# Performance work log

Hardware: AMD Instinct MI355X
Metric: run time of the kernel (lower is better)

The kernel has to match this reference:

```python
import jax, jax.numpy as jnp
import numpy as np
import math

D_MODEL = 768
N_HEADS = 12
D_HEAD = D_MODEL // N_HEADS


def setup_inputs() -> dict:
    key = jax.random.key(0)
    ks = jax.random.split(key, 5)
    x = jax.random.normal(ks[0], (2, 4096, D_MODEL), dtype=jnp.float32)
    s = 1.0 / math.sqrt(D_MODEL)
    W_qkv = jax.random.normal(ks[1], (D_MODEL, 3 * D_MODEL), dtype=jnp.float32) * s
    b_qkv = jnp.zeros((3 * D_MODEL,), dtype=jnp.float32)
    W_out = jax.random.normal(ks[2], (D_MODEL, D_MODEL), dtype=jnp.float32) * s
    b_out = jnp.zeros((D_MODEL,), dtype=jnp.float32)
    return {"x": x, "W_qkv": W_qkv, "b_qkv": b_qkv, "W_out": W_out, "b_out": b_out}


def reference(x, W_qkv, b_qkv, W_out, b_out):
    B, T, C = x.shape
    H, Dh = N_HEADS, D_HEAD
    qkv = x @ W_qkv + b_qkv                      # [B,T,3C]
    q, k, v = jnp.split(qkv, 3, axis=-1)
    q = q.reshape(B, T, H, Dh).transpose(0, 2, 1, 3)  # [B,H,T,Dh]
    k = k.reshape(B, T, H, Dh).transpose(0, 2, 1, 3)
    v = v.reshape(B, T, H, Dh).transpose(0, 2, 1, 3)
    att = jnp.einsum('bhqd,bhkd->bhqk', q, k) * (1.0 / math.sqrt(Dh))
    causal = jnp.tril(jnp.ones((T, T), dtype=bool))
    att = jnp.where(causal, att, -jnp.inf)
    att = jax.nn.softmax(att, axis=-1)
    out = jnp.einsum('bhqk,bhkd->bhqd', att, v)  # [B,H,T,Dh]
    out = out.transpose(0, 2, 1, 3).reshape(B, T, C)
    return out @ W_out + b_out
```

## Files before the change

### kernel.cpp

```cpp
#include <hip/hip_runtime.h>
#include <hip/hip_bf16.h>
#include <cstdint>

#define NH 12
#define DH 64
#define TSEQ 4096
#define BATCH 2
#define CDIM 768
#define MROWS (BATCH*TSEQ)

typedef __bf16 bf16x8 __attribute__((ext_vector_type(8)));
typedef __bf16 bf16x4 __attribute__((ext_vector_type(4)));
typedef bf16x8 bf16x8_a __attribute__((may_alias));
typedef bf16x4 bf16x4_a __attribute__((may_alias));
typedef float f32x4 __attribute__((ext_vector_type(4)));

__device__ __forceinline__ uint16_t f2bu(float f) {
  uint32_t u = __float_as_uint(f);
  u += 0x7fffu + ((u >> 16) & 1u);
  return (uint16_t)(u >> 16);
}

__device__ __forceinline__ float bu2f(uint16_t x) {
  return __uint_as_float(((uint32_t)x) << 16);
}

__device__ __forceinline__ void gload_lds16(const void* g, void* l) {
  __builtin_amdgcn_global_load_lds(
      (const __attribute__((address_space(1))) void*)g,
      (__attribute__((address_space(3))) void*)l, 16, 0, 0);
}

__global__ void cast_f32_bf16(const float* __restrict__ in, uint16_t* __restrict__ out, int n4) {
  int i = blockIdx.x * blockDim.x + threadIdx.x;
  int stride = gridDim.x * blockDim.x;
  for (; i < n4; i += stride) {
    float4 v = ((const float4*)in)[i];
    ushort4 o;
    o.x = f2bu(v.x); o.y = f2bu(v.y); o.z = f2bu(v.z); o.w = f2bu(v.w);
    ((ushort4*)out)[i] = o;
  }
}

__global__ void transpose_cast(const float* __restrict__ w, uint16_t* __restrict__ wt, int K, int N) {
  __shared__ float tile[32][33];
  int kb = blockIdx.x * 32, nb = blockIdx.y * 32;
  int tx = threadIdx.x & 31, ty = threadIdx.x >> 5;
  #pragma unroll
  for (int r = ty; r < 32; r += 8) tile[r][tx] = w[(size_t)(kb + r) * N + nb + tx];
  __syncthreads();
  #pragma unroll
  for (int r = ty; r < 32; r += 8) wt[(size_t)(nb + r) * K + kb + tx] = f2bu(tile[tx][r]);
}

__global__ __launch_bounds__(256) void gemm_qkv(
    const uint16_t* __restrict__ A, const uint16_t* __restrict__ Bt,
    const float* __restrict__ bias,
    uint16_t* __restrict__ q, uint16_t* __restrict__ k, uint16_t* __restrict__ v,
    int N, int K) {
  __shared__ uint16_t As[128 * 32];
  __shared__ uint16_t Bs[128 * 32];
  int tid = threadIdx.x;
  int w = tid >> 6, l = tid & 63;
  int lg = l >> 4, lr = l & 15;
  int mb = blockIdx.x * 128, nb = blockIdx.y * 128;
  int wr = (w >> 1) * 64, wc = (w & 1) * 64;
  f32x4 acc[4][4] = {};
  int srow = tid >> 2, scol = (tid & 3) * 8;
  const uint16_t* Ag = A + (size_t)(mb + srow) * K + scol;
  const uint16_t* Bg = Bt + (size_t)(nb + srow) * K + scol;
  char* AsB = (char*)As + (size_t)w * 1024;
  char* BsB = (char*)Bs + (size_t)w * 1024;
  size_t rowskip = (size_t)64 * K;
  for (int kb = 0; kb < K; kb += 32) {
    __syncthreads();
    gload_lds16(Ag + kb, AsB);
    gload_lds16(Ag + kb + rowskip, AsB + 4096);
    gload_lds16(Bg + kb, BsB);
    gload_lds16(Bg + kb + rowskip, BsB + 4096);
    __syncthreads();
    bf16x8 af[4], bfr[4];
    #pragma unroll
    for (int i = 0; i < 4; ++i)
      af[i] = *(const bf16x8_a*)(const void*)(As + (wr + i * 16 + lr) * 32 + lg * 8);
    #pragma unroll
    for (int i = 0; i < 4; ++i)
      bfr[i] = *(const bf16x8_a*)(const void*)(Bs + (wc + i * 16 + lr) * 32 + lg * 8);
    #pragma unroll
    for (int mi = 0; mi < 4; ++mi)
      #pragma unroll
      for (int ni = 0; ni < 4; ++ni)
        acc[mi][ni] = __builtin_amdgcn_mfma_f32_16x16x32_bf16(af[mi], bfr[ni], acc[mi][ni], 0, 0, 0);
  }
  #pragma unroll
  for (int mi = 0; mi < 4; ++mi) {
    #pragma unroll
    for (int ni = 0; ni < 4; ++ni) {
      int gm0 = mb + wr + mi * 16 + lg * 4;
      int gn = nb + wc + ni * 16 + lr;
      int which = gn / CDIM;
      int cc = gn - which * CDIM;
      int hh = cc >> 6, d = cc & 63;
      float bs = bias[gn];
      if (which == 2) {
        int b0 = gm0 >> 12, t0 = gm0 & 4095;
        ushort4 pk;
        pk.x = f2bu(acc[mi][ni][0] + bs);
        pk.y = f2bu(acc[mi][ni][1] + bs);
        pk.z = f2bu(acc[mi][ni][2] + bs);
        pk.w = f2bu(acc[mi][ni][3] + bs);
        *(ushort4*)&v[(((size_t)(b0 * NH + hh)) * DH + d) * TSEQ + t0] = pk;
      } else {
        uint16_t* dst = which ? k : q;
        float sc = which ? 1.0f : 0.1803368801111204f;
        #pragma unroll
        for (int j = 0; j < 4; ++j) {
          int gm = gm0 + j;
          int bb = gm >> 12, t = gm & 4095;
          float val = (acc[mi][ni][j] + bs) * sc;
          dst[(((size_t)(bb * NH + hh)) * TSEQ + t) * DH + d] = f2bu(val);
        }
      }
    }
  }
}

__global__ __launch_bounds__(256) void gemm_out(
    const uint16_t* __restrict__ A, const uint16_t* __restrict__ Bt,
    const float* __restrict__ bias, float* __restrict__ outf, int N, int K) {
  __shared__ uint16_t As[128 * 32];
  __shared__ uint16_t Bs[64 * 32];
  int tid = threadIdx.x;
  int w = tid >> 6, l = tid & 63;
  int lg = l >> 4, lr = l & 15;
  int mb = blockIdx.x * 128, nb = blockIdx.y * 64;
  int wr = w * 32;
  f32x4 acc[2][4] = {};
  int srow = tid >> 2, scol = (tid & 3) * 8;
  const uint16_t* Ag = A + (size_t)(mb + srow) * K + scol;
  const uint16_t* Bg = Bt + (size_t)(nb + srow) * K + scol;
  char* AsB = (char*)As + (size_t)w * 1024;
  char* BsB = (char*)Bs + (size_t)w * 1024;
  size_t rowskip = (size_t)64 * K;
  for (int kb = 0; kb < K; kb += 32) {
    __syncthreads();
    gload_lds16(Ag + kb, AsB);
    gload_lds16(Ag + kb + rowskip, AsB + 4096);
    gload_lds16(Bg + kb, BsB);
    __syncthreads();
    bf16x8 af[2], bfr[4];
    #pragma unroll
    for (int i = 0; i < 2; ++i)
      af[i] = *(const bf16x8_a*)(const void*)(As + (wr + i * 16 + lr) * 32 + lg * 8);
    #pragma unroll
    for (int i = 0; i < 4; ++i)
      bfr[i] = *(const bf16x8_a*)(const void*)(Bs + (i * 16 + lr) * 32 + lg * 8);
    #pragma unroll
    for (int mi = 0; mi < 2; ++mi)
      #pragma unroll
      for (int ni = 0; ni < 4; ++ni)
        acc[mi][ni] = __builtin_amdgcn_mfma_f32_16x16x32_bf16(af[mi], bfr[ni], acc[mi][ni], 0, 0, 0);
  }
  #pragma unroll
  for (int mi = 0; mi < 2; ++mi) {
    #pragma unroll
    for (int ni = 0; ni < 4; ++ni) {
      #pragma unroll
      for (int j = 0; j < 4; ++j) {
        int gm = mb + wr + mi * 16 + lg * 4 + j;
        int gn = nb + ni * 16 + lr;
        outf[(size_t)gm * N + gn] = acc[mi][ni][j] + bias[gn];
      }
    }
  }
}

__device__ __forceinline__ int lbase_qt(int qt) {
  return (qt < 22) ? (qt - 11) * 2 : 22 + (qt - 22) * 3;
}
__device__ __forceinline__ int ebase_qt(int qt) {
  return (qt < 22) ? (qt - 11) : 11 + (qt - 22) * 2;
}

__global__ __launch_bounds__(256) void attn_part(
    const uint16_t* __restrict__ Q, const uint16_t* __restrict__ K,
    const uint16_t* __restrict__ Vt, uint16_t* __restrict__ O,
    uint16_t* __restrict__ Pbuf, float* __restrict__ Pl) {
  int gid = blockIdx.x;
  int widx = gid / 24, bh = gid - widx * 24;
  int qt, c, nch;
  if (widx < 30) { qt = 31 - widx / 3; c = widx % 3; nch = 3; }
  else if (widx < 52) { int u = widx - 30; qt = 21 - (u >> 1); c = u & 1; nch = 2; }
  else { qt = 62 - widx; c = 0; nch = 1; }
  int ntile = 2 * qt + 2;
  int L = (ntile + nch - 1) / nch;
  int t0 = c * L;
  int t1 = min(ntile - 1, t0 + L - 1);

  int b = bh / NH, hd = bh - b * NH;
  size_t base = (size_t)bh * TSEQ * DH;
  int tid = threadIdx.x, w = tid >> 6, lane = tid & 63;
  int lg = lane >> 4, lr = lane & 15;
  __shared__ __align__(16) uint16_t Ks[64 * 64];
  __shared__ __align__(16) uint16_t Vs[64 * 64];
  __shared__ uint16_t Ps[4][16 * 64];
  char* pw = (char*)Ps[w];
  int srow = tid >> 3;
  int schunk = (tid & 7) ^ (srow & 7);
  const uint16_t* Kg0 = K + base + (size_t)srow * DH + schunk * 8;
  const uint16_t* Vg0 = Vt + base + (size_t)srow * TSEQ + schunk * 8;
  char* KsB = (char*)Ks + w * 1024;
  char* VsB = (char*)Vs + w * 1024;
  int swzA = (lg ^ (lr & 7)) << 4;
  int swzB = swzA ^ 64;

  int qb = qt * 128;
  int qgA = qb + w * 16 + lr;
  int qgB = qgA + 64;
  bf16x8 qA0 = *(const bf16x8_a*)(const void*)(Q + base + (size_t)qgA * DH + lg * 8);
  bf16x8 qA1 = *(const bf16x8_a*)(const void*)(Q + base + (size_t)qgA * DH + 32 + lg * 8);
  bf16x8 qB0 = *(const bf16x8_a*)(const void*)(Q + base + (size_t)qgB * DH + lg * 8);
  bf16x8 qB1 = *(const bf16x8_a*)(const void*)(Q + base + (size_t)qgB * DH + 32 + lg * 8);
  f32x4 oA[4] = {}, oB[4] = {};
  float lA = 0.f, lB = 0.f;
  int lg4 = lg * 4;
  int pofs = (lg & 1) * 8;

  for (int t = t0; t <= t1; ++t) {
    __syncthreads();
    {
      const uint16_t* kg_ = Kg0 + (size_t)t * (64 * DH);
      const uint16_t* vg_ = Vg0 + (size_t)t * 64;
      gload_lds16(kg_,           KsB);
      gload_lds16(kg_ + 32 * DH, KsB + 4096);
      gload_lds16(vg_,                     VsB);
      gload_lds16(vg_ + (size_t)32 * TSEQ, VsB + 4096);
    }
    __syncthreads();
    bool doA = (t <= 2 * qt);
    int kb0 = t * 64;
    f32x4 sA[4], sB[4];
    __builtin_amdgcn_s_setprio(1);
    #pragma unroll
    for (int ni = 0; ni < 4; ++ni) {
      const char* kbp = (const char*)Ks + (ni * 16 + lr) * 128;
      bf16x8 kf0 = *(const bf16x8_a*)(kbp + swzA);
      bf16x8 kf1 = *(const bf16x8_a*)(kbp + swzB);
      f32x4 s = {};
      s = __builtin_amdgcn_mfma_f32_16x16x32_bf16(kf0, qB0, s, 0, 0, 0);
      s = __builtin_amdgcn_mfma_f32_16x16x32_bf16(kf1, qB1, s, 0, 0, 0);
      sB[ni] = s;
      if (doA) {
        f32x4 sa = {};
        sa = __builtin_amdgcn_mfma_f32_16x16x32_bf16(kf0, qA0, sa, 0, 0, 0);
        sa = __builtin_amdgcn_mfma_f32_16x16x32_bf16(kf1, qA1, sa, 0, 0, 0);
        sA[ni] = sa;
      }
    }
    __builtin_amdgcn_s_setprio(0);
    bf16x8 pfA0, pfA1;
    if (doA) {
      if (t == 2 * qt) {
        int thr = qgA - kb0 - lg4;
        #pragma unroll
        for (int ni = 0; ni < 4; ++ni)
          #pragma unroll
          for (int j = 0; j < 4; ++j)
            sA[ni][j] = (16 * ni + j <= thr) ? sA[ni][j] : -1e30f;
      }
      #pragma unroll
      for (int ni = 0; ni < 4; ++ni) {
        float p0 = __builtin_amdgcn_exp2f(sA[ni][0]);
        float p1 = __builtin_amdgcn_exp2f(sA[ni][1]);
        float p2 = __builtin_amdgcn_exp2f(sA[ni][2]);
        float p3 = __builtin_amdgcn_exp2f(sA[ni][3]);
        lA += (p0 + p1) + (p2 + p3);
        bf16x4 pk;
        pk[0] = (__bf16)p0; pk[1] = (__bf16)p1; pk[2] = (__bf16)p2; pk[3] = (__bf16)p3;
        int chunkc = (2 * ni + (lg >> 1)) ^ (lr & 7);
        *(bf16x4_a*)(pw + lr * 128 + chunkc * 16 + pofs) = pk;
      }
      pfA0 = *(const bf16x8_a*)(pw + lr * 128 + swzA);
      pfA1 = *(const bf16x8_a*)(pw + lr * 128 + swzB);
    }
    {
      if (t == 2 * qt + 1) {
        int thr = qgB - kb0 - lg4;
        #pragma unroll
        for (int ni = 0; ni < 4; ++ni)
          #pragma unroll
          for (int j = 0; j < 4; ++j)
            sB[ni][j] = (16 * ni + j <= thr) ? sB[ni][j] : -1e30f;
      }
      #pragma unroll
      for (int ni = 0; ni < 4; ++ni) {
        float p0 = __builtin_amdgcn_exp2f(sB[ni][0]);
        float p1 = __builtin_amdgcn_exp2f(sB[ni][1]);
        float p2 = __builtin_amdgcn_exp2f(sB[ni][2]);
        float p3 = __builtin_amdgcn_exp2f(sB[ni][3]);
        lB += (p0 + p1) + (p2 + p3);
        bf16x4 pk;
        pk[0] = (__bf16)p0; pk[1] = (__bf16)p1; pk[2] = (__bf16)p2; pk[3] = (__bf16)p3;
        int chunkc = (2 * ni + (lg >> 1)) ^ (lr & 7);
        *(bf16x4_a*)(pw + lr * 128 + chunkc * 16 + pofs) = pk;
      }
    }
    bf16x8 pfB0 = *(const bf16x8_a*)(pw + lr * 128 + swzA);
    bf16x8 pfB1 = *(const bf16x8_a*)(pw + lr * 128 + swzB);
    __builtin_amdgcn_s_setprio(1);
    #pragma unroll
    for (int nd = 0; nd < 4; ++nd) {
      const char* vb = (const char*)Vs + (nd * 16 + lr) * 128;
      bf16x8 vf0 = *(const bf16x8_a*)(vb + swzA);
      bf16x8 vf1 = *(const bf16x8_a*)(vb + swzB);
      oB[nd] = __builtin_amdgcn_mfma_f32_16x16x32_bf16(pfB0, vf0, oB[nd], 0, 0, 0);
      oB[nd] = __builtin_amdgcn_mfma_f32_16x16x32_bf16(pfB1, vf1, oB[nd], 0, 0, 0);
      if (doA) {
        oA[nd] = __builtin_amdgcn_mfma_f32_16x16x32_bf16(pfA0, vf0, oA[nd], 0, 0, 0);
        oA[nd] = __builtin_amdgcn_mfma_f32_16x16x32_bf16(pfA1, vf1, oA[nd], 0, 0, 0);
      }
    }
    __builtin_amdgcn_s_setprio(0);
  }

  lA += __shfl_xor(lA, 16, 64); lA += __shfl_xor(lA, 32, 64);
  lB += __shfl_xor(lB, 16, 64); lB += __shfl_xor(lB, 32, 64);
  if (nch == 1) {
    float riA = 1.0f / lA, riB = 1.0f / lB;
    #pragma unroll
    for (int j = 0; j < 4; ++j) {
      float rvA = __shfl(riA, (lane & 48) | (lg4 + j), 64);
      float rvB = __shfl(riB, (lane & 48) | (lg4 + j), 64);
      int tA = qb + w * 16 + lg4 + j;
      size_t pA = (size_t)(b * TSEQ + tA) * CDIM + hd * DH + lr;
      size_t pB = pA + (size_t)64 * CDIM;
      #pragma unroll
      for (int nd = 0; nd < 4; ++nd) {
        O[pA + nd * 16] = f2bu(oA[nd][j] * rvA);
        O[pB + nd * 16] = f2bu(oB[nd][j] * rvB);
      }
    }
  } else {
    float* pl = Pl + (size_t)(bh * 64 + lbase_qt(qt) + c) * 128;
    if (lane < 16) {
      pl[w * 16 + lane] = lA;
      pl[64 + w * 16 + lane] = lB;
    }
    if (c == 0) {
      #pragma unroll
      for (int j = 0; j < 4; ++j) {
        int tA = qb + w * 16 + lg4 + j;
        size_t pA = (size_t)(b * TSEQ + tA) * CDIM + hd * DH + lr;
        size_t pB = pA + (size_t)64 * CDIM;
        #pragma unroll
        for (int nd = 0; nd < 4; ++nd) {
          O[pA + nd * 16] = f2bu(oA[nd][j]);
          O[pB + nd * 16] = f2bu(oB[nd][j]);
        }
      }
    } else {
      uint16_t* Pb = Pbuf + (size_t)(bh * 31 + ebase_qt(qt) + (c - 1)) * 8192;
      #pragma unroll
      for (int j = 0; j < 4; ++j) {
        int qlA = w * 16 + lg4 + j;
        #pragma unroll
        for (int nd = 0; nd < 4; ++nd) {
          Pb[qlA * 64 + nd * 16 + lr] = f2bu(oA[nd][j]);
          Pb[(64 + qlA) * 64 + nd * 16 + lr] = f2bu(oB[nd][j]);
        }
      }
    }
  }
}

__global__ __launch_bounds__(256) void attn_reduce(
    const uint16_t* __restrict__ Pbuf, const float* __restrict__ Pl,
    uint16_t* __restrict__ O) {
  int rid = blockIdx.x;
  int bh = rid / 21, qt = 11 + (rid - bh * 21);
  int nch = (qt >= 22) ? 3 : 2;
  int b = bh / NH, hd = bh - b * NH;
  int tid = threadIdx.x;
  const float* pl = Pl + (size_t)(bh * 64 + lbase_qt(qt)) * 128;
  const uint16_t* pb = Pbuf + (size_t)(bh * 31 + ebase_qt(qt)) * 8192;
  #pragma unroll
  for (int it = 0; it < 8; ++it) {
    int idx = it * 256 + tid;
    int q = idx >> 4, dq = idx & 15;
    float lsum = pl[q] + pl[128 + q];
    if (nch == 3) lsum += pl[256 + q];
    float linv = 1.0f / lsum;
    int t = qt * 128 + q;
    size_t po = (size_t)(b * TSEQ + t) * CDIM + hd * DH + dq * 4;
    ushort4 ov = *(const ushort4*)&O[po];
    ushort4 pv = *(const ushort4*)&pb[q * 64 + dq * 4];
    float s0 = bu2f(ov.x) + bu2f(pv.x);
    float s1 = bu2f(ov.y) + bu2f(pv.y);
    float s2 = bu2f(ov.z) + bu2f(pv.z);
    float s3 = bu2f(ov.w) + bu2f(pv.w);
    if (nch == 3) {
      ushort4 pv2 = *(const ushort4*)&pb[8192 + q * 64 + dq * 4];
      s0 += bu2f(pv2.x); s1 += bu2f(pv2.y); s2 += bu2f(pv2.z); s3 += bu2f(pv2.w);
    }
    ushort4 o;
    o.x = f2bu(s0 * linv); o.y = f2bu(s1 * linv);
    o.z = f2bu(s2 * linv); o.w = f2bu(s3 * linv);
    *(ushort4*)&O[po] = o;
  }
}

extern "C" void kernel_launch(void* const* d_in, const int* in_sizes, int n_in,
                              void* d_out, int out_size, void* d_ws, size_t ws_size,
                              hipStream_t stream) {
  const float* x    = (const float*)d_in[0];
  const float* Wqkv = (const float*)d_in[1];
  const float* bqkv = (const float*)d_in[2];
  const float* Wout = (const float*)d_in[3];
  const float* bout = (const float*)d_in[4];
  float* out = (float*)d_out;
  char* ws = (char*)d_ws;

  uint16_t* Xb    = (uint16_t*)(ws + 0);
  uint16_t* Wqkvt = (uint16_t*)(ws + 12582912);
  uint16_t* Woutt = (uint16_t*)(ws + 16121856);
  uint16_t* Qb    = (uint16_t*)(ws + 17301504);
  uint16_t* Kb    = (uint16_t*)(ws + 29884416);
  uint16_t* Vtb   = (uint16_t*)(ws + 42467328);
  uint16_t* Ob    = (uint16_t*)(ws + 55050240);
  uint16_t* Pbuf  = Xb;
  float*    Pl    = (float*)Wqkvt;

  cast_f32_bf16<<<2048, 256, 0, stream>>>(x, Xb, (MROWS * CDIM) / 4);
  transpose_cast<<<dim3(24, 72), 256, 0, stream>>>(Wqkv, Wqkvt, 768, 2304);
  transpose_cast<<<dim3(24, 24), 256, 0, stream>>>(Wout, Woutt, 768, 768);
  gemm_qkv<<<dim3(64, 18), 256, 0, stream>>>(Xb, Wqkvt, bqkv, Qb, Kb, Vtb, 2304, 768);
  attn_part<<<1512, 256, 0, stream>>>(Qb, Kb, Vtb, Ob, Pbuf, Pl);
  attn_reduce<<<504, 256, 0, stream>>>(Pbuf, Pl, Ob);
  gemm_out<<<dim3(64, 12), 256, 0, stream>>>(Ob, Woutt, bout, out, 768, 768);
}
```

Baseline: 176.0 us.

## Keep softmax probabilities in registers by permuting K rows to match the MFMA layout

The K tile rows read for the QK^T MFMA are permuted, and the LDS swizzle is changed to match, so that each lane's score outputs line up with the A-operand layout of the PV MFMA. The probabilities can then be packed straight into bf16x8 fragments in registers instead of being written to a per-wave LDS buffer and read back. This removes the Ps shared buffer, its LDS writes and reads, and the related latency. It also adjusts the causal mask offsets and the V read swizzle, and it only stays correct if the row permutation and the swizzle remain consistent.

Measured after the change: 176.9 us. No clear change (+0.5%).

```diff
diff --git a/kernel.cpp b/kernel.cpp
--- a/kernel.cpp
+++ b/kernel.cpp
@@ -14,6 +14,7 @@
 typedef bf16x8 bf16x8_a __attribute__((may_alias));
 typedef bf16x4 bf16x4_a __attribute__((may_alias));
 typedef float f32x4 __attribute__((ext_vector_type(4)));
+typedef uint32_t u32;
 
 __device__ __forceinline__ uint16_t f2bu(float f) {
   uint32_t u = __float_as_uint(f);
@@ -23,6 +24,18 @@
 
 __device__ __forceinline__ float bu2f(uint16_t x) {
   return __uint_as_float(((uint32_t)x) << 16);
+}
+
+__device__ __forceinline__ u32 pkbf(float a, float b) {
+  union { __bf16 h[2]; u32 u; } t;
+  t.h[0] = (__bf16)a; t.h[1] = (__bf16)b;
+  return t.u;
+}
+
+__device__ __forceinline__ bf16x8 mkfrag(u32 a, u32 b, u32 c, u32 d) {
+  union { u32 u[4]; bf16x8 v; } t;
+  t.u[0] = a; t.u[1] = b; t.u[2] = c; t.u[3] = d;
+  return t.v;
 }
 
 __device__ __forceinline__ void gload_lds16(const void* g, void* l) {
@@ -203,16 +216,16 @@
   int lg = lane >> 4, lr = lane & 15;
   __shared__ __align__(16) uint16_t Ks[64 * 64];
   __shared__ __align__(16) uint16_t Vs[64 * 64];
-  __shared__ uint16_t Ps[4][16 * 64];
-  char* pw = (char*)Ps[w];
   int srow = tid >> 3;
-  int schunk = (tid & 7) ^ (srow & 7);
+  int schunk = (tid & 7) ^ (srow & 7) ^ (((srow >> 3) & 1) << 2);
   const uint16_t* Kg0 = K + base + (size_t)srow * DH + schunk * 8;
   const uint16_t* Vg0 = Vt + base + (size_t)srow * TSEQ + schunk * 8;
   char* KsB = (char*)Ks + w * 1024;
   char* VsB = (char*)Vs + w * 1024;
-  int swzA = (lg ^ (lr & 7)) << 4;
-  int swzB = swzA ^ 64;
+
+  int rb = ((lr >> 2) << 3) | (lr & 3);
+  int ck0 = lg ^ (lr & 3) ^ (((lr >> 2) & 1) << 2);
+  int cv0 = lg ^ (lr & 7) ^ (((lr >> 3) & 1) << 2);
 
   int qb = qt * 128;
   int qgA = qb + w * 16 + lr;
@@ -223,8 +236,7 @@
   bf16x8 qB1 = *(const bf16x8_a*)(const void*)(Q + base + (size_t)qgB * DH + 32 + lg * 8);
   f32x4 oA[4] = {}, oB[4] = {};
   float lA = 0.f, lB = 0.f;
-  int lg4 = lg * 4;
-  int pofs = (lg & 1) * 8;
+  int lg4 = lg * 4, lg8 = lg * 8;
 
   for (int t = t0; t <= t1; ++t) {
     __syncthreads();
@@ -243,9 +255,11 @@
     __builtin_amdgcn_s_setprio(1);
     #pragma unroll
     for (int ni = 0; ni < 4; ++ni) {
-      const char* kbp = (const char*)Ks + (ni * 16 + lr) * 128;
-      bf16x8 kf0 = *(const bf16x8_a*)(kbp + swzA);
-      bf16x8 kf1 = *(const bf16x8_a*)(kbp + swzB);
+      int row = rb + ((ni & 1) << 2) + ((ni >> 1) << 5);
+      int ch = ck0 ^ ((ni & 1) << 2);
+      const char* kbp = (const char*)Ks + row * 128;
+      bf16x8 kf0 = *(const bf16x8_a*)(kbp + ch * 16);
+      bf16x8 kf1 = *(const bf16x8_a*)(kbp + (ch ^ 4) * 16);
       f32x4 s = {};
       s = __builtin_amdgcn_mfma_f32_16x16x32_bf16(kf0, qB0, s, 0, 0, 0);
       s = __builtin_amdgcn_mfma_f32_16x16x32_bf16(kf1, qB1, s, 0, 0, 0);
@@ -261,13 +275,16 @@
     bf16x8 pfA0, pfA1;
     if (doA) {
       if (t == 2 * qt) {
-        int thr = qgA - kb0 - lg4;
+        int thr = qgA - kb0 - lg8;
         #pragma unroll
-        for (int ni = 0; ni < 4; ++ni)
+        for (int ni = 0; ni < 4; ++ni) {
+          int off = ((ni & 1) << 2) + ((ni >> 1) << 5);
           #pragma unroll
           for (int j = 0; j < 4; ++j)
-            sA[ni][j] = (16 * ni + j <= thr) ? sA[ni][j] : -1e30f;
-      }
+            sA[ni][j] = (off + j <= thr) ? sA[ni][j] : -1e30f;
+        }
+      }
+      u32 ca[8];
       #pragma unroll
       for (int ni = 0; ni < 4; ++ni) {
         float p0 = __builtin_amdgcn_exp2f(sA[ni][0]);
@@ -275,23 +292,25 @@
         float p2 = __builtin_amdgcn_exp2f(sA[ni][2]);
         float p3 = __builtin_amdgcn_exp2f(sA[ni][3]);
         lA += (p0 + p1) + (p2 + p3);
-        bf16x4 pk;
-        pk[0] = (__bf16)p0; pk[1] = (__bf16)p1; pk[2] = (__bf16)p2; pk[3] = (__bf16)p3;
-        int chunkc = (2 * ni + (lg >> 1)) ^ (lr & 7);
-        *(bf16x4_a*)(pw + lr * 128 + chunkc * 16 + pofs) = pk;
-      }
-      pfA0 = *(const bf16x8_a*)(pw + lr * 128 + swzA);
-      pfA1 = *(const bf16x8_a*)(pw + lr * 128 + swzB);
-    }
+        ca[2 * ni] = pkbf(p0, p1);
+        ca[2 * ni + 1] = pkbf(p2, p3);
+      }
+      pfA0 = mkfrag(ca[0], ca[1], ca[2], ca[3]);
+      pfA1 = mkfrag(ca[4], ca[5], ca[6], ca[7]);
+    }
+    bf16x8 pfB0, pfB1;
     {
       if (t == 2 * qt + 1) {
-        int thr = qgB - kb0 - lg4;
+        int thr = qgB - kb0 - lg8;
         #pragma unroll
-        for (int ni = 0; ni < 4; ++ni)
+        for (int ni = 0; ni < 4; ++ni) {
+          int off = ((ni & 1) << 2) + ((ni >> 1) << 5);
           #pragma unroll
           for (int j = 0; j < 4; ++j)
-            sB[ni][j] = (16 * ni + j <= thr) ? sB[ni][j] : -1e30f;
-      }
+            sB[ni][j] = (off + j <= thr) ? sB[ni][j] : -1e30f;
+        }
+      }
+      u32 cb[8];
       #pragma unroll
       for (int ni = 0; ni < 4; ++ni) {
         float p0 = __builtin_amdgcn_exp2f(sB[ni][0]);
@@ -299,20 +318,18 @@
         float p2 = __builtin_amdgcn_exp2f(sB[ni][2]);
         float p3 = __builtin_amdgcn_exp2f(sB[ni][3]);
         lB += (p0 + p1) + (p2 + p3);
-        bf16x4 pk;
-        pk[0] = (__bf16)p0; pk[1] = (__bf16)p1; pk[2] = (__bf16)p2; pk[3] = (__bf16)p3;
-        int chunkc = (2 * ni + (lg >> 1)) ^ (lr & 7);
-        *(bf16x4_a*)(pw + lr * 128 + chunkc * 16 + pofs) = pk;
-      }
-    }
-    bf16x8 pfB0 = *(const bf16x8_a*)(pw + lr * 128 + swzA);
-    bf16x8 pfB1 = *(const bf16x8_a*)(pw + lr * 128 + swzB);
+        cb[2 * ni] = pkbf(p0, p1);
+        cb[2 * ni + 1] = pkbf(p2, p3);
+      }
+      pfB0 = mkfrag(cb[0], cb[1], cb[2], cb[3]);
+      pfB1 = mkfrag(cb[4], cb[5], cb[6], cb[7]);
+    }
     __builtin_amdgcn_s_setprio(1);
     #pragma unroll
     for (int nd = 0; nd < 4; ++nd) {
       const char* vb = (const char*)Vs + (nd * 16 + lr) * 128;
-      bf16x8 vf0 = *(const bf16x8_a*)(vb + swzA);
-      bf16x8 vf1 = *(const bf16x8_a*)(vb + swzB);
+      bf16x8 vf0 = *(const bf16x8_a*)(vb + cv0 * 16);
+      bf16x8 vf1 = *(const bf16x8_a*)(vb + (cv0 ^ 4) * 16);
       oB[nd] = __builtin_amdgcn_mfma_f32_16x16x32_bf16(pfB0, vf0, oB[nd], 0, 0, 0);
       oB[nd] = __builtin_amdgcn_mfma_f32_16x16x32_bf16(pfB1, vf1, oB[nd], 0, 0, 0);
       if (doA) {
```
